# Kernel optimization log

Hardware: AMD Instinct MI355X
Metric: run time of the kernel (lower is better)

Reference implementation:

```python
import jax, jax.numpy as jnp
import numpy as np

LEAK = 0.01  # F.leaky_relu default negative_slope


def projection(p, cam, res):
    # Weak-perspective projection to normalized [-1,1] image coords.
    # cam = [s, tx, ty]; p [B,N,3] -> [B,N,2]
    s = cam[:, 0][:, None, None]
    t = cam[:, None, 1:3]
    return s * (p[..., :2] + t)


def grid_sample_points(im_feat, pts):
    # Bilinear grid_sample with align_corners=True, zeros padding,
    # specialized to a [B,N,1,2] point grid (matches points.unsqueeze(2)).
    # im_feat [B,C,H,W], pts [B,N,2] in [-1,1] -> [B,C,N]
    B, C, H, W = im_feat.shape
    N = pts.shape[1]
    x = (pts[..., 0] + 1.0) * 0.5 * (W - 1)
    y = (pts[..., 1] + 1.0) * 0.5 * (H - 1)
    x0 = jnp.floor(x)
    y0 = jnp.floor(y)
    x1 = x0 + 1.0
    y1 = y0 + 1.0
    wx1 = x - x0
    wx0 = 1.0 - wx1
    wy1 = y - y0
    wy0 = 1.0 - wy1
    feat_flat = im_feat.reshape(B, C, H * W)

    def gather(xi, yi, w):
        valid = (xi >= 0) & (xi <= W - 1) & (yi >= 0) & (yi <= H - 1)
        xc = jnp.clip(xi, 0, W - 1).astype(jnp.int32)
        yc = jnp.clip(yi, 0, H - 1).astype(jnp.int32)
        idx = (yc * W + xc)[:, None, :]  # [B,1,N]
        g = jnp.take_along_axis(feat_flat, jnp.broadcast_to(idx, (B, C, N)), axis=2)
        return g * (w * valid.astype(w.dtype))[:, None, :]

    return (gather(x0, y0, wx0 * wy0) + gather(x1, y0, wx1 * wy0)
            + gather(x0, y1, wx0 * wy1) + gather(x1, y1, wx1 * wy1))


def reduce_dim(feat, W0, b0, W1, b1, W2, b2):
    # feat [B,C0,N]; Conv1d kernel_size=1 == channel matmul.
    def conv1x1(x, W, b):
        return jnp.einsum('oc,bcn->bon', W, x) + b[None, :, None]

    y = jax.nn.leaky_relu(conv1x1(feat, W0, b0), LEAK)
    y = jax.nn.leaky_relu(conv1x1(jnp.concatenate([y, feat], axis=1), W1, b1), LEAK)
    y = conv1x1(jnp.concatenate([y, feat], axis=1), W2, b2)
    y = jax.nn.relu(y)  # last_op
    return y.reshape(y.shape[0], -1)  # [B, C_p*N]


def setup_inputs() -> dict:
    key = jax.random.key(0)
    ks = jax.random.split(key, 9)
    B, N, C, H, Wd = 64, 431, 256, 56, 56
    dims = [256, 128, 64, 5]
    p = jax.random.normal(ks[0], (B, N, 3), jnp.float32)
    cam = jax.random.uniform(ks[1], (B, 3), jnp.float32)
    s_feat = jax.random.normal(ks[2], (B, C, H, Wd), jnp.float32)
    W0 = jax.random.normal(ks[3], (dims[1], dims[0]), jnp.float32) * 0.02
    b0 = jnp.zeros((dims[1],), jnp.float32)
    W1 = jax.random.normal(ks[4], (dims[2], dims[1] + dims[0]), jnp.float32) * 0.02
    b1 = jnp.zeros((dims[2],), jnp.float32)
    W2 = jax.random.normal(ks[5], (dims[3], dims[2] + dims[0]), jnp.float32) * 0.02
    b2 = jnp.zeros((dims[3],), jnp.float32)
    return {"p": p, "cam": cam, "s_feat": s_feat,
            "W0": W0, "b0": b0, "W1": W1, "b1": b1, "W2": W2, "b2": b2,
            "res": 224}


def reference(p, cam, s_feat, W0, b0, W1, b1, W2, b2, res):
    p2d = projection(p, cam, res)                 # [B,N,2]
    point_feat = grid_sample_points(s_feat, p2d)  # [B,C_s,N]
    return reduce_dim(point_feat, W0, b0, W1, b1, W2, b2)  # [B, C_p*N]
```

## Files before the change

kernel.cpp:

```cpp
#include <hip/hip_runtime.h>


#define B_   64
#define N_   431
#define C_   256
#define H_   56
#define W_   56
#define HW_  3136
#define PPB  16
#define NT_  27
#define NPAD (NT_ * PPB)

#define Y0S  136
#define Y1S  72

typedef __attribute__((ext_vector_type(8))) short short8;
typedef __attribute__((ext_vector_type(4))) float f32x4;

__device__ __forceinline__ ushort f2bf(float f) {
    unsigned u = __float_as_uint(f);
    u += 0x7fffu + ((u >> 16) & 1u);
    return (ushort)(u >> 16);
}

#define WTOT (128 * 256 + 64 * 384 + 16 * 320)
#define GB_  (B_ * 64)

__global__ __launch_bounds__(256, 2) void gather_kernel(
    const float* __restrict__ p,
    const float* __restrict__ cam,
    const float* __restrict__ sfeat,
    const float* __restrict__ W0,
    const float* __restrict__ W1,
    const float* __restrict__ W2,
    ushort* __restrict__ feat,
    ushort* __restrict__ W0b,
    ushort* __restrict__ W1b,
    ushort* __restrict__ W2p)
{
    const int bx = blockIdx.x;
    if (bx >= GB_) {
        const int t0 = (bx - GB_) * 256 + threadIdx.x;
        for (int i = t0; i < WTOT; i += 8 * 256) {
            if (i < 128 * 256) {
                W0b[i] = f2bf(W0[i]);
            } else if (i < 128 * 256 + 64 * 384) {
                const int j = i - 128 * 256;
                W1b[j] = f2bf(W1[j]);
            } else {
                const int j = i - (128 * 256 + 64 * 384);
                const int r = j / 320, c = j - r * 320;
                W2p[j] = (r < 5) ? f2bf(W2[r * 320 + c]) : (ushort)0;
            }
        }
        return;
    }

    __shared__ float planes[4][HW_];
    __shared__ int   pidx[NPAD][4];
    __shared__ float pw[NPAD][4];

    const int b  = bx >> 6;
    const int c0 = (bx & 63) * 4;
    const int t  = threadIdx.x;

    #pragma unroll
    for (int j = 0; j < 4; ++j) {
        const float4* __restrict__ src =
            (const float4*)(sfeat + ((size_t)b * C_ + c0 + j) * HW_);
        for (int k = t; k < HW_ / 4; k += 256)
            *(float4*)&planes[j][k * 4] = src[k];
    }

    {
        const float s  = cam[b * 3 + 0];
        const float tx = cam[b * 3 + 1];
        const float ty = cam[b * 3 + 2];
        for (int n = t; n < NPAD; n += 256) {
            int   i00 = 0, i10 = 0, i01 = 0, i11 = 0;
            float w00 = 0.f, w10 = 0.f, w01 = 0.f, w11 = 0.f;
            if (n < N_) {
                const float px = p[((size_t)b * N_ + n) * 3 + 0];
                const float py = p[((size_t)b * N_ + n) * 3 + 1];
                const float x = (s * (px + tx) + 1.f) * 0.5f * (float)(W_ - 1);
                const float y = (s * (py + ty) + 1.f) * 0.5f * (float)(H_ - 1);
                const float x0f = floorf(x), y0f = floorf(y);
                const float wx1 = x - x0f, wx0 = 1.f - wx1;
                const float wy1 = y - y0f, wy0 = 1.f - wy1;
                const int ix0 = (int)x0f, iy0 = (int)y0f;
                const int ix1 = ix0 + 1,  iy1 = iy0 + 1;
                const bool vx0 = (ix0 >= 0) & (ix0 <= W_ - 1);
                const bool vx1 = (ix1 >= 0) & (ix1 <= W_ - 1);
                const bool vy0 = (iy0 >= 0) & (iy0 <= H_ - 1);
                const bool vy1 = (iy1 >= 0) & (iy1 <= H_ - 1);
                const int cx0 = min(max(ix0, 0), W_ - 1);
                const int cx1 = min(max(ix1, 0), W_ - 1);
                const int cy0 = min(max(iy0, 0), H_ - 1);
                const int cy1 = min(max(iy1, 0), H_ - 1);
                w00 = (vx0 & vy0) ? wx0 * wy0 : 0.f;
                w10 = (vx1 & vy0) ? wx1 * wy0 : 0.f;
                w01 = (vx0 & vy1) ? wx0 * wy1 : 0.f;
                w11 = (vx1 & vy1) ? wx1 * wy1 : 0.f;
                i00 = cy0 * W_ + cx0;  i10 = cy0 * W_ + cx1;
                i01 = cy1 * W_ + cx0;  i11 = cy1 * W_ + cx1;
            }
            pidx[n][0] = i00; pidx[n][1] = i10; pidx[n][2] = i01; pidx[n][3] = i11;
            pw[n][0] = w00;   pw[n][1] = w10;   pw[n][2] = w01;   pw[n][3] = w11;
        }
    }
    __syncthreads();

    for (int n = t; n < NPAD; n += 256) {
        const int   i00 = pidx[n][0], i10 = pidx[n][1], i01 = pidx[n][2], i11 = pidx[n][3];
        const float w00 = pw[n][0],   w10 = pw[n][1],   w01 = pw[n][2],   w11 = pw[n][3];
        ushort4 r;
        r.x = f2bf(w00 * planes[0][i00] + w10 * planes[0][i10] + w01 * planes[0][i01] + w11 * planes[0][i11]);
        r.y = f2bf(w00 * planes[1][i00] + w10 * planes[1][i10] + w01 * planes[1][i01] + w11 * planes[1][i11]);
        r.z = f2bf(w00 * planes[2][i00] + w10 * planes[2][i10] + w01 * planes[2][i01] + w11 * planes[2][i11]);
        r.w = f2bf(w00 * planes[3][i00] + w10 * planes[3][i10] + w01 * planes[3][i01] + w11 * planes[3][i11]);
        *(ushort4*)(feat + ((size_t)b * NPAD + n) * C_ + c0) = r;
    }
}

__global__ __launch_bounds__(256, 4) void mlp_kernel(
    const ushort* __restrict__ feat,
    const ushort* __restrict__ W0b,
    const float* __restrict__ b0,
    const ushort* __restrict__ W1b,
    const float* __restrict__ b1,
    const ushort* __restrict__ W2p,
    const float* __restrict__ b2,
    float* __restrict__ out)
{
    __shared__ ushort y0_s[PPB * Y0S];
    __shared__ ushort y1_s[PPB * Y1S];

    const int tid  = threadIdx.x;
    const int w    = tid >> 6;
    const int l    = tid & 63;
    const int m    = l & 15;
    const int q    = l >> 4;
    const int tile = blockIdx.x;
    const int b    = blockIdx.y;
    const int n0   = tile * PPB;

    const ushort* __restrict__ fb =
        feat + (((size_t)b * NT_ + tile) * PPB + m) * C_ + 8 * q;
    short8 af[8];
    #pragma unroll
    for (int ks = 0; ks < 8; ++ks) af[ks] = *(const short8*)(fb + 32 * ks);

    {
        f32x4 acc0 = {0.f, 0.f, 0.f, 0.f};
        f32x4 acc1 = {0.f, 0.f, 0.f, 0.f};
        const ushort* __restrict__ wr0 = W0b + ((size_t)(2 * w) * 16 + m) * 256 + 8 * q;
        const ushort* __restrict__ wr1 = wr0 + 16 * 256;
        #pragma unroll
        for (int ks = 0; ks < 8; ++ks) {
            const short8 w0 = *(const short8*)(wr0 + 32 * ks);
            const short8 w1 = *(const short8*)(wr1 + 32 * ks);
            acc0 = __builtin_amdgcn_mfma_f32_16x16x32_bf16(af[ks], w0, acc0, 0, 0, 0);
            acc1 = __builtin_amdgcn_mfma_f32_16x16x32_bf16(af[ks], w1, acc1, 0, 0, 0);
        }
        const int o0 = (2 * w) * 16 + m, o1 = o0 + 16;
        const float bias0 = b0[o0], bias1 = b0[o1];
        #pragma unroll
        for (int r = 0; r < 4; ++r) {
            float v0 = acc0[r] + bias0; v0 = (v0 > 0.f) ? v0 : 0.01f * v0;
            float v1 = acc1[r] + bias1; v1 = (v1 > 0.f) ? v1 : 0.01f * v1;
            y0_s[(q * 4 + r) * Y0S + o0] = f2bf(v0);
            y0_s[(q * 4 + r) * Y0S + o1] = f2bf(v1);
        }
    }
    __syncthreads();

    {
        f32x4 acc = {0.f, 0.f, 0.f, 0.f};
        const ushort* __restrict__ wr = W1b + ((size_t)w * 16 + m) * 384 + 8 * q;
        #pragma unroll
        for (int ks = 0; ks < 4; ++ks) {
            const short8 a  = *(const short8*)(y0_s + m * Y0S + 32 * ks + 8 * q);
            const short8 bb = *(const short8*)(wr + 32 * ks);
            acc = __builtin_amdgcn_mfma_f32_16x16x32_bf16(a, bb, acc, 0, 0, 0);
        }
        #pragma unroll
        for (int ks = 4; ks < 12; ++ks) {
            const short8 bb = *(const short8*)(wr + 32 * ks);
            acc = __builtin_amdgcn_mfma_f32_16x16x32_bf16(af[ks - 4], bb, acc, 0, 0, 0);
        }
        const int o = w * 16 + m;
        const float bias = b1[o];
        #pragma unroll
        for (int r = 0; r < 4; ++r) {
            float v = acc[r] + bias; v = (v > 0.f) ? v : 0.01f * v;
            y1_s[(q * 4 + r) * Y1S + o] = f2bf(v);
        }
    }
    __syncthreads();

    if (w == 0) {
        f32x4 acc = {0.f, 0.f, 0.f, 0.f};
        const ushort* __restrict__ wr = W2p + (size_t)m * 320 + 8 * q;
        #pragma unroll
        for (int ks = 0; ks < 2; ++ks) {
            const short8 a  = *(const short8*)(y1_s + m * Y1S + 32 * ks + 8 * q);
            const short8 bb = *(const short8*)(wr + 32 * ks);
            acc = __builtin_amdgcn_mfma_f32_16x16x32_bf16(a, bb, acc, 0, 0, 0);
        }
        #pragma unroll
        for (int ks = 2; ks < 10; ++ks) {
            const short8 bb = *(const short8*)(wr + 32 * ks);
            acc = __builtin_amdgcn_mfma_f32_16x16x32_bf16(af[ks - 2], bb, acc, 0, 0, 0);
        }
        if (m < 5) {
            const float bias = b2[m];
            #pragma unroll
            for (int r = 0; r < 4; ++r) {
                const int n = n0 + q * 4 + r;
                if (n < N_) {
                    float v = acc[r] + bias;
                    out[((size_t)b * 5 + m) * N_ + n] = (v > 0.f) ? v : 0.f;
                }
            }
        }
    }
}

__global__ __launch_bounds__(256, 4) void maf_fallback_kernel(
    const float* __restrict__ p, const float* __restrict__ cam,
    const float* __restrict__ sfeat,
    const float* __restrict__ W0, const float* __restrict__ b0,
    const float* __restrict__ W1, const float* __restrict__ b1,
    const float* __restrict__ W2, const float* __restrict__ b2,
    float* __restrict__ out)
{
    __shared__ float feat_s[PPB][C_ + 4];
    __shared__ float y0_s[PPB][128 + 4];
    __shared__ float y1_s[PPB][64 + 4];

    const int tid = threadIdx.x;
    const int b   = blockIdx.y;
    const int n0  = blockIdx.x * PPB;
    const float s  = cam[b * 3 + 0];
    const float tx = cam[b * 3 + 1];
    const float ty = cam[b * 3 + 2];
    {
        const int c = tid;
        const float* __restrict__ fb = sfeat + ((size_t)b * C_ + c) * HW_;
        for (int pp = 0; pp < PPB; ++pp) {
            const int n = n0 + pp;
            float val = 0.f;
            if (n < N_) {
                const float px = p[((size_t)b * N_ + n) * 3 + 0];
                const float py = p[((size_t)b * N_ + n) * 3 + 1];
                const float x = (s * (px + tx) + 1.f) * 0.5f * (float)(W_ - 1);
                const float y = (s * (py + ty) + 1.f) * 0.5f * (float)(H_ - 1);
                const float x0f = floorf(x), y0f = floorf(y);
                const float wx1 = x - x0f, wx0 = 1.f - wx1;
                const float wy1 = y - y0f, wy0 = 1.f - wy1;
                const int ix0 = (int)x0f, iy0 = (int)y0f;
                const int ix1 = ix0 + 1,  iy1 = iy0 + 1;
                const bool vx0 = (ix0 >= 0) & (ix0 <= W_ - 1);
                const bool vx1 = (ix1 >= 0) & (ix1 <= W_ - 1);
                const bool vy0 = (iy0 >= 0) & (iy0 <= H_ - 1);
                const bool vy1 = (iy1 >= 0) & (iy1 <= H_ - 1);
                const int cx0 = min(max(ix0, 0), W_ - 1);
                const int cx1 = min(max(ix1, 0), W_ - 1);
                const int cy0 = min(max(iy0, 0), H_ - 1);
                const int cy1 = min(max(iy1, 0), H_ - 1);
                const float w00 = (vx0 & vy0) ? wx0 * wy0 : 0.f;
                const float w10 = (vx1 & vy0) ? wx1 * wy0 : 0.f;
                const float w01 = (vx0 & vy1) ? wx0 * wy1 : 0.f;
                const float w11 = (vx1 & vy1) ? wx1 * wy1 : 0.f;
                val = w00 * fb[cy0 * W_ + cx0] + w10 * fb[cy0 * W_ + cx1]
                    + w01 * fb[cy1 * W_ + cx0] + w11 * fb[cy1 * W_ + cx1];
            }
            feat_s[pp][c] = val;
        }
    }
    __syncthreads();
    {
        const int o = tid & 127, pg = tid >> 7, p0 = pg * 8;
        const float* __restrict__ wr = W0 + (size_t)o * 256;
        float acc[8] = {0, 0, 0, 0, 0, 0, 0, 0};
        for (int k = 0; k < 256; k += 4) {
            const float4 w = *(const float4*)(wr + k);
            for (int i = 0; i < 8; ++i) {
                const float4 f = *(const float4*)&feat_s[p0 + i][k];
                acc[i] += w.x * f.x + w.y * f.y + w.z * f.z + w.w * f.w;
            }
        }
        const float bias = b0[o];
        for (int i = 0; i < 8; ++i) {
            const float v = acc[i] + bias;
            y0_s[p0 + i][o] = (v > 0.f) ? v : 0.01f * v;
        }
    }
    __syncthreads();
    {
        const int o = tid & 63, pg = tid >> 6, p0 = pg * 4;
        const float* __restrict__ wr = W1 + (size_t)o * 384;
        float acc[4] = {0, 0, 0, 0};
        for (int k = 0; k < 128; k += 4) {
            const float4 w = *(const float4*)(wr + k);
            for (int i = 0; i < 4; ++i) {
                const float4 f = *(const float4*)&y0_s[p0 + i][k];
                acc[i] += w.x * f.x + w.y * f.y + w.z * f.z + w.w * f.w;
            }
        }
        for (int k = 0; k < 256; k += 4) {
            const float4 w = *(const float4*)(wr + 128 + k);
            for (int i = 0; i < 4; ++i) {
                const float4 f = *(const float4*)&feat_s[p0 + i][k];
                acc[i] += w.x * f.x + w.y * f.y + w.z * f.z + w.w * f.w;
            }
        }
        const float bias = b1[o];
        for (int i = 0; i < 4; ++i) {
            const float v = acc[i] + bias;
            y1_s[p0 + i][o] = (v > 0.f) ? v : 0.01f * v;
        }
    }
    __syncthreads();
    if (tid < 80) {
        const int o = tid >> 4, pp = tid & 15;
        const float* __restrict__ wr = W2 + (size_t)o * 320;
        float acc = 0.f;
        for (int k = 0; k < 64; k += 4) {
            const float4 w = *(const float4*)(wr + k);
            const float4 f = *(const float4*)&y1_s[pp][k];
            acc += w.x * f.x + w.y * f.y + w.z * f.z + w.w * f.w;
        }
        for (int k = 0; k < 256; k += 4) {
            const float4 w = *(const float4*)(wr + 64 + k);
            const float4 f = *(const float4*)&feat_s[pp][k];
            acc += w.x * f.x + w.y * f.y + w.z * f.z + w.w * f.w;
        }
        const int n = n0 + pp;
        if (n < N_) {
            float v = acc + b2[o];
            out[((size_t)b * 5 + o) * N_ + n] = (v > 0.f) ? v : 0.f;
        }
    }
}

extern "C" void kernel_launch(void* const* d_in, const int* in_sizes, int n_in,
                              void* d_out, int out_size, void* d_ws, size_t ws_size,
                              hipStream_t stream) {
    const float* p     = (const float*)d_in[0];
    const float* cam   = (const float*)d_in[1];
    const float* sfeat = (const float*)d_in[2];
    const float* W0    = (const float*)d_in[3];
    const float* b0    = (const float*)d_in[4];
    const float* W1    = (const float*)d_in[5];
    const float* b1    = (const float*)d_in[6];
    const float* W2    = (const float*)d_in[7];
    const float* b2    = (const float*)d_in[8];
    float* out = (float*)d_out;

    const size_t feat_elems = (size_t)B_ * NPAD * C_;
    size_t off = feat_elems;
    const size_t w0_off = off; off += 128 * 256;
    const size_t w1_off = off; off += 64 * 384;
    const size_t w2_off = off; off += 16 * 320;
    const size_t need = off * sizeof(ushort);

    if (ws_size >= need) {
        ushort* feat = (ushort*)d_ws;
        ushort* W0b  = feat + w0_off;
        ushort* W1b  = feat + w1_off;
        ushort* W2p  = feat + w2_off;
        gather_kernel<<<GB_ + 8, 256, 0, stream>>>(
            p, cam, sfeat, W0, W1, W2, feat, W0b, W1b, W2p);
        mlp_kernel<<<dim3(NT_, B_), 256, 0, stream>>>(
            feat, W0b, b0, W1b, b1, W2p, b2, out);
    } else {
        maf_fallback_kernel<<<dim3(NT_, B_), 256, 0, stream>>>(
            p, cam, sfeat, W0, b0, W1, b1, W2, b2, out);
    }
}
```

Before: 377.8 us.

## Pack feature planes as bf16 pairs in LDS and relayout intermediate feat buffer

The gather kernel now stores the four channel planes in shared memory as packed bf16 pairs (two uint planes), which halves LDS use. It also computes bilinear indices and weights inline rather than staging them in shared arrays. Launch bounds go from 2 to 6 blocks per CU to raise occupancy for the memory-bound plane loads. The intermediate feat buffer is relaid out as [B][channel-group][N][4], giving contiguous writes from the gather, and the MLP kernel's fragment loads are adjusted to match. Quantising the planes to bf16 before interpolation adds a little rounding error.

```diff
diff --git a/kernel.cpp b/kernel.cpp
--- a/kernel.cpp
+++ b/kernel.cpp
@@ -22,11 +22,16 @@
     u += 0x7fffu + ((u >> 16) & 1u);
     return (ushort)(u >> 16);
 }
+__device__ __forceinline__ uint pack2(float lo, float hi) {
+    return (uint)f2bf(lo) | ((uint)f2bf(hi) << 16);
+}
+__device__ __forceinline__ float lo16(uint u) { return __uint_as_float(u << 16); }
+__device__ __forceinline__ float hi16(uint u) { return __uint_as_float(u & 0xffff0000u); }
 
 #define WTOT (128 * 256 + 64 * 384 + 16 * 320)
 #define GB_  (B_ * 64)
 
-__global__ __launch_bounds__(256, 2) void gather_kernel(
+__global__ __launch_bounds__(256, 6) void gather_kernel(
     const float* __restrict__ p,
     const float* __restrict__ cam,
     const float* __restrict__ sfeat,
@@ -56,69 +61,76 @@
         return;
     }
 
-    __shared__ float planes[4][HW_];
-    __shared__ int   pidx[NPAD][4];
-    __shared__ float pw[NPAD][4];
+    __shared__ uint plane01[HW_];
+    __shared__ uint plane23[HW_];
 
     const int b  = bx >> 6;
-    const int c0 = (bx & 63) * 4;
+    const int cg = bx & 63;
+    const int c0 = cg * 4;
     const int t  = threadIdx.x;
 
-    #pragma unroll
-    for (int j = 0; j < 4; ++j) {
-        const float4* __restrict__ src =
-            (const float4*)(sfeat + ((size_t)b * C_ + c0 + j) * HW_);
-        for (int k = t; k < HW_ / 4; k += 256)
-            *(float4*)&planes[j][k * 4] = src[k];
-    }
-
-    {
-        const float s  = cam[b * 3 + 0];
-        const float tx = cam[b * 3 + 1];
-        const float ty = cam[b * 3 + 2];
-        for (int n = t; n < NPAD; n += 256) {
-            int   i00 = 0, i10 = 0, i01 = 0, i11 = 0;
-            float w00 = 0.f, w10 = 0.f, w01 = 0.f, w11 = 0.f;
-            if (n < N_) {
-                const float px = p[((size_t)b * N_ + n) * 3 + 0];
-                const float py = p[((size_t)b * N_ + n) * 3 + 1];
-                const float x = (s * (px + tx) + 1.f) * 0.5f * (float)(W_ - 1);
-                const float y = (s * (py + ty) + 1.f) * 0.5f * (float)(H_ - 1);
-                const float x0f = floorf(x), y0f = floorf(y);
-                const float wx1 = x - x0f, wx0 = 1.f - wx1;
-                const float wy1 = y - y0f, wy0 = 1.f - wy1;
-                const int ix0 = (int)x0f, iy0 = (int)y0f;
-                const int ix1 = ix0 + 1,  iy1 = iy0 + 1;
-                const bool vx0 = (ix0 >= 0) & (ix0 <= W_ - 1);
-                const bool vx1 = (ix1 >= 0) & (ix1 <= W_ - 1);
-                const bool vy0 = (iy0 >= 0) & (iy0 <= H_ - 1);
-                const bool vy1 = (iy1 >= 0) & (iy1 <= H_ - 1);
-                const int cx0 = min(max(ix0, 0), W_ - 1);
-                const int cx1 = min(max(ix1, 0), W_ - 1);
-                const int cy0 = min(max(iy0, 0), H_ - 1);
-                const int cy1 = min(max(iy1, 0), H_ - 1);
-                w00 = (vx0 & vy0) ? wx0 * wy0 : 0.f;
-                w10 = (vx1 & vy0) ? wx1 * wy0 : 0.f;
-                w01 = (vx0 & vy1) ? wx0 * wy1 : 0.f;
-                w11 = (vx1 & vy1) ? wx1 * wy1 : 0.f;
-                i00 = cy0 * W_ + cx0;  i10 = cy0 * W_ + cx1;
-                i01 = cy1 * W_ + cx0;  i11 = cy1 * W_ + cx1;
-            }
-            pidx[n][0] = i00; pidx[n][1] = i10; pidx[n][2] = i01; pidx[n][3] = i11;
-            pw[n][0] = w00;   pw[n][1] = w10;   pw[n][2] = w01;   pw[n][3] = w11;
-        }
-    }
-    __syncthreads();
+    {
+        const float4* __restrict__ s0 = (const float4*)(sfeat + ((size_t)b * C_ + c0 + 0) * HW_);
+        const float4* __restrict__ s1 = (const float4*)(sfeat + ((size_t)b * C_ + c0 + 1) * HW_);
+        const float4* __restrict__ s2 = (const float4*)(sfeat + ((size_t)b * C_ + c0 + 2) * HW_);
+        const float4* __restrict__ s3 = (const float4*)(sfeat + ((size_t)b * C_ + c0 + 3) * HW_);
+        for (int k = t; k < HW_ / 4; k += 256) {
+            const float4 a = s0[k], bb = s1[k];
+            uint4 u01;
+            u01.x = pack2(a.x, bb.x); u01.y = pack2(a.y, bb.y);
+            u01.z = pack2(a.z, bb.z); u01.w = pack2(a.w, bb.w);
+            *(uint4*)&plane01[k * 4] = u01;
+            const float4 c = s2[k], d = s3[k];
+            uint4 u23;
+            u23.x = pack2(c.x, d.x); u23.y = pack2(c.y, d.y);
+            u23.z = pack2(c.z, d.z); u23.w = pack2(c.w, d.w);
+            *(uint4*)&plane23[k * 4] = u23;
+        }
+    }
+    __syncthreads();
+
+    const float s  = cam[b * 3 + 0];
+    const float tx = cam[b * 3 + 1];
+    const float ty = cam[b * 3 + 2];
+    ushort* __restrict__ fdst = feat + ((size_t)b * 64 + cg) * NPAD * 4;
 
     for (int n = t; n < NPAD; n += 256) {
-        const int   i00 = pidx[n][0], i10 = pidx[n][1], i01 = pidx[n][2], i11 = pidx[n][3];
-        const float w00 = pw[n][0],   w10 = pw[n][1],   w01 = pw[n][2],   w11 = pw[n][3];
+        int   i00 = 0, i10 = 0, i01 = 0, i11 = 0;
+        float w00 = 0.f, w10 = 0.f, w01 = 0.f, w11 = 0.f;
+        if (n < N_) {
+            const float px = p[((size_t)b * N_ + n) * 3 + 0];
+            const float py = p[((size_t)b * N_ + n) * 3 + 1];
+            const float x = (s * (px + tx) + 1.f) * 0.5f * (float)(W_ - 1);
+            const float y = (s * (py + ty) + 1.f) * 0.5f * (float)(H_ - 1);
+            const float x0f = floorf(x), y0f = floorf(y);
+            const float wx1 = x - x0f, wx0 = 1.f - wx1;
+            const float wy1 = y - y0f, wy0 = 1.f - wy1;
+            const int ix0 = (int)x0f, iy0 = (int)y0f;
+            const int ix1 = ix0 + 1,  iy1 = iy0 + 1;
+            const bool vx0 = (ix0 >= 0) & (ix0 <= W_ - 1);
+            const bool vx1 = (ix1 >= 0) & (ix1 <= W_ - 1);
+            const bool vy0 = (iy0 >= 0) & (iy0 <= H_ - 1);
+            const bool vy1 = (iy1 >= 0) & (iy1 <= H_ - 1);
+            const int cx0 = min(max(ix0, 0), W_ - 1);
+            const int cx1 = min(max(ix1, 0), W_ - 1);
+            const int cy0 = min(max(iy0, 0), H_ - 1);
+            const int cy1 = min(max(iy1, 0), H_ - 1);
+            w00 = (vx0 & vy0) ? wx0 * wy0 : 0.f;
+            w10 = (vx1 & vy0) ? wx1 * wy0 : 0.f;
+            w01 = (vx0 & vy1) ? wx0 * wy1 : 0.f;
+            w11 = (vx1 & vy1) ? wx1 * wy1 : 0.f;
+            i00 = cy0 * W_ + cx0;  i10 = cy0 * W_ + cx1;
+            i01 = cy1 * W_ + cx0;  i11 = cy1 * W_ + cx1;
+        }
+        const uint a00 = plane01[i00], a10 = plane01[i10], a01 = plane01[i01], a11 = plane01[i11];
+        const uint c00 = plane23[i00], c10 = plane23[i10], c01 = plane23[i01], c11 = plane23[i11];
+        const float v0 = w00 * lo16(a00) + w10 * lo16(a10) + w01 * lo16(a01) + w11 * lo16(a11);
+        const float v1 = w00 * hi16(a00) + w10 * hi16(a10) + w01 * hi16(a01) + w11 * hi16(a11);
+        const float v2 = w00 * lo16(c00) + w10 * lo16(c10) + w01 * lo16(c01) + w11 * lo16(c11);
+        const float v3 = w00 * hi16(c00) + w10 * hi16(c10) + w01 * hi16(c01) + w11 * hi16(c11);
         ushort4 r;
-        r.x = f2bf(w00 * planes[0][i00] + w10 * planes[0][i10] + w01 * planes[0][i01] + w11 * planes[0][i11]);
-        r.y = f2bf(w00 * planes[1][i00] + w10 * planes[1][i10] + w01 * planes[1][i01] + w11 * planes[1][i11]);
-        r.z = f2bf(w00 * planes[2][i00] + w10 * planes[2][i10] + w01 * planes[2][i01] + w11 * planes[2][i11]);
-        r.w = f2bf(w00 * planes[3][i00] + w10 * planes[3][i10] + w01 * planes[3][i01] + w11 * planes[3][i11]);
-        *(ushort4*)(feat + ((size_t)b * NPAD + n) * C_ + c0) = r;
+        r.x = f2bf(v0); r.y = f2bf(v1); r.z = f2bf(v2); r.w = f2bf(v3);
+        *(ushort4*)(fdst + (size_t)n * 4) = r;
     }
 }
 
@@ -143,12 +155,18 @@
     const int tile = blockIdx.x;
     const int b    = blockIdx.y;
     const int n0   = tile * PPB;
-
-    const ushort* __restrict__ fb =
-        feat + (((size_t)b * NT_ + tile) * PPB + m) * C_ + 8 * q;
+    const int n    = n0 + m;
+
+    const ushort* __restrict__ fb = feat + (size_t)b * 64 * NPAD * 4;
     short8 af[8];
     #pragma unroll
-    for (int ks = 0; ks < 8; ++ks) af[ks] = *(const short8*)(fb + 32 * ks);
+    for (int ks = 0; ks < 8; ++ks) {
+        const int cg0 = 8 * ks + 2 * q;
+        union { short8 v; uint2 u[2]; } tmp;
+        tmp.u[0] = *(const uint2*)(fb + ((size_t)cg0 * NPAD + n) * 4);
+        tmp.u[1] = *(const uint2*)(fb + ((size_t)(cg0 + 1) * NPAD + n) * 4);
+        af[ks] = tmp.v;
+    }
 
     {
         f32x4 acc0 = {0.f, 0.f, 0.f, 0.f};
@@ -216,10 +234,10 @@
             const float bias = b2[m];
             #pragma unroll
             for (int r = 0; r < 4; ++r) {
-                const int n = n0 + q * 4 + r;
-                if (n < N_) {
+                const int nn = n0 + q * 4 + r;
+                if (nn < N_) {
                     float v = acc[r] + bias;
-                    out[((size_t)b * 5 + m) * N_ + n] = (v > 0.f) ? v : 0.f;
+                    out[((size_t)b * 5 + m) * N_ + nn] = (v > 0.f) ? v : 0.f;
                 }
             }
         }
@@ -358,7 +376,7 @@
     const float* b2    = (const float*)d_in[8];
     float* out = (float*)d_out;
 
-    const size_t feat_elems = (size_t)B_ * NPAD * C_;
+    const size_t feat_elems = (size_t)B_ * 64 * NPAD * 4;
     size_t off = feat_elems;
     const size_t w0_off = off; off += 128 * 256;
     const size_t w1_off = off; off += 64 * 384;
```

New measurement: 336.3 us. 11.0% less time.
